# Performance work log

Hardware: AMD Instinct MI355X
Metric: run time of the kernel (lower is better)

The kernel has to match this reference:

```python
import jax, jax.numpy as jnp
import numpy as np

B, S, H, L = 8, 4096, 768, 256   # batch, seq_len, hidden_size, num_lines (= line_ids.max()+1)
ATT_HID = 1024                    # attention MLP hidden dim from nn.Linear(hidden,1024)


def setup_inputs() -> dict:
    key = jax.random.key(0)
    k0, k1, k2, k3 = jax.random.split(key, 4)
    token_hidden = jax.random.normal(k0, (B, S, H), dtype=jnp.float32)
    line_ids = jax.random.randint(k1, (B, S), 0, L)  # all valid; -1 would mark invalid
    W1 = jax.random.normal(k2, (H, ATT_HID), dtype=jnp.float32) * 0.02
    b1 = jnp.zeros((ATT_HID,), jnp.float32)
    W2 = jax.random.normal(k3, (ATT_HID, 1), dtype=jnp.float32) * 0.02
    b2 = jnp.zeros((1,), jnp.float32)
    return {"token_hidden": token_hidden, "line_ids": line_ids,
            "W1": W1, "b1": b1, "W2": W2, "b2": b2}


def reference(token_hidden, line_ids, W1, b1, W2, b2):
    b, s, h = token_hidden.shape
    num_lines = L
    n_seg = b * num_lines + 1  # last segment is a dump slot for invalid (-1) tokens

    # attention scores: Linear -> tanh -> Linear, squeeze(-1)  [b, s]
    scores = (jnp.tanh(token_hidden @ W1 + b1) @ W2 + b2)[..., 0]

    valid = (line_ids >= 0).reshape(-1)                                   # [b*s]
    seg = jnp.where(line_ids >= 0,
                    jnp.arange(b)[:, None] * num_lines + line_ids,
                    b * num_lines).reshape(-1)                            # [b*s]
    s_flat = jnp.where(valid, scores.reshape(-1), -jnp.inf)

    # segment-wise stable softmax
    m = jax.ops.segment_max(s_flat, seg, num_segments=n_seg)
    m = jnp.where(jnp.isfinite(m), m, 0.0)  # empty segments -> safe 0
    e = jnp.where(valid, jnp.exp(scores.reshape(-1) - m[seg]), 0.0)
    denom = jax.ops.segment_sum(e, seg, num_segments=n_seg)
    w = e / jnp.maximum(denom[seg], 1e-20)                                # [b*s]

    # weighted sum of tokens per (batch, line) segment
    feats = jax.ops.segment_sum(token_hidden.reshape(-1, h) * w[:, None],
                                seg, num_segments=n_seg)
    line_features = feats[: b * num_lines].reshape(b, num_lines, h)

    counts = jax.ops.segment_sum(valid.astype(jnp.float32), seg, num_segments=n_seg)
    line_mask = counts[: b * num_lines].reshape(b, num_lines) > 0
    return line_features, line_mask
```

## Files before the change

kernel.cpp:

```cpp
#include <hip/hip_runtime.h>
#include <hip/hip_bf16.h>
#include <string.h>

#define M_TOK 32768
#define H_DIM 768
#define AH    1024
#define NSEG  2048
#define LCAP  192
#define CONV_BLOCKS 12288

typedef __attribute__((ext_vector_type(8))) __bf16 bf16x8;
typedef __attribute__((ext_vector_type(4))) float f32x4;

__device__ __forceinline__ float tanh_fast(float x) {
  float e = __expf(2.0f * x);
  return 1.0f - 2.0f * __builtin_amdgcn_rcpf(e + 1.0f);
}

__device__ __forceinline__ float bf2f(unsigned short u) {
  unsigned int v = (unsigned int)u << 16;
  float f;
  memcpy(&f, &v, 4);
  return f;
}

__global__ __launch_bounds__(256) void prep_kernel(
    const float* __restrict__ W1, __hip_bfloat16* __restrict__ W1t,
    const float4* __restrict__ X4, uint4* __restrict__ Xb4) {
  __shared__ float tile[32][33];
  if (blockIdx.x < 768) {
    int nt = blockIdx.x & 31, ktile = blockIdx.x >> 5;
    int n0 = nt * 32, k0 = ktile * 32;
    int tx = threadIdx.x & 31, ty = threadIdx.x >> 5;
    for (int r = ty; r < 32; r += 8)
      tile[r][tx] = W1[(size_t)(k0 + r) * AH + n0 + tx];
    __syncthreads();
    for (int r = ty; r < 32; r += 8)
      W1t[(size_t)(n0 + r) * H_DIM + k0 + tx] = __float2bfloat16(tile[tx][r]);
  } else {
    int i = (blockIdx.x - 768) * 256 + threadIdx.x;
    float4 v0 = X4[i * 2];
    float4 v1 = X4[i * 2 + 1];
    __hip_bfloat16 h[8] = {
        __float2bfloat16(v0.x), __float2bfloat16(v0.y),
        __float2bfloat16(v0.z), __float2bfloat16(v0.w),
        __float2bfloat16(v1.x), __float2bfloat16(v1.y),
        __float2bfloat16(v1.z), __float2bfloat16(v1.w)};
    uint4 p;
    memcpy(&p, h, 16);
    Xb4[i] = p;
  }
}

__global__ __launch_bounds__(256) void attn_score_kernel(
    const __hip_bfloat16* __restrict__ Xbg,
    const __hip_bfloat16* __restrict__ W1tg, const float* __restrict__ b1g,
    const float* __restrict__ W2g, float* __restrict__ scores2) {
  __shared__ __align__(16) __bf16 As[128 * 64];
  __shared__ __align__(16) __bf16 Bs[128 * 64];

  const int tid = threadIdx.x;
  const int bid = blockIdx.x;
  const int xcd = bid & 7;
  const int s   = bid >> 3;
  const int m0  = (xcd * 32 + (s >> 3)) * 128;
  const int nt  = s & 7;
  const int n0  = nt * 128;
  const int lane = tid & 63;
  const int wave = tid >> 6;
  const int wm   = (wave >> 1) * 64;
  const int wn   = (wave & 1) * 64;
  const int ml   = lane & 15;
  const int gsw  = lane & 7;

  const __bf16* Xb = (const __bf16*)Xbg;
  const __bf16* W  = (const __bf16*)W1tg;

  const int srow = tid >> 3;
  const int scol = ((tid & 7) ^ (srow & 7)) * 8;

  f32x4 acc[4][4];
#pragma unroll
  for (int i = 0; i < 4; i++)
#pragma unroll
    for (int j = 0; j < 4; j++) acc[i][j] = (f32x4)0.f;

  for (int kt = 0; kt < H_DIM; kt += 64) {
#pragma unroll
    for (int p = 0; p < 4; ++p) {
      const __bf16* ga = Xb + (size_t)(m0 + p * 32 + srow) * H_DIM + kt + scol;
      __builtin_amdgcn_global_load_lds(
          (const __attribute__((address_space(1))) void*)ga,
          (__attribute__((address_space(3))) void*)&As[p * 2048 + tid * 8],
          16, 0, 0);
      const __bf16* gb = W + (size_t)(n0 + p * 32 + srow) * H_DIM + kt + scol;
      __builtin_amdgcn_global_load_lds(
          (const __attribute__((address_space(1))) void*)gb,
          (__attribute__((address_space(3))) void*)&Bs[p * 2048 + tid * 8],
          16, 0, 0);
    }
    __syncthreads();

#pragma unroll
    for (int c = 0; c < 2; ++c) {
      const int gq = c * 4 + (lane >> 4);
      const int gp = (gq ^ gsw) * 8;
      bf16x8 af[4], bf[4];
#pragma unroll
      for (int i = 0; i < 4; i++)
        af[i] = *(const bf16x8*)&As[(wm + i * 16 + ml) * 64 + gp];
#pragma unroll
      for (int j = 0; j < 4; j++)
        bf[j] = *(const bf16x8*)&Bs[(wn + j * 16 + ml) * 64 + gp];

#pragma unroll
      for (int i = 0; i < 4; i++)
#pragma unroll
        for (int j = 0; j < 4; j++)
          acc[i][j] = __builtin_amdgcn_mfma_f32_16x16x32_bf16(af[i], bf[j],
                                                              acc[i][j], 0, 0, 0);
    }
    __syncthreads();
  }

  float b1v[4], w2v[4];
#pragma unroll
  for (int j = 0; j < 4; j++) {
    int n = n0 + wn + j * 16 + ml;
    b1v[j] = b1g[n];
    w2v[j] = W2g[n];
  }
  const int q4 = (lane >> 4) * 4;
  float tval[4][4];
#pragma unroll
  for (int i = 0; i < 4; i++) {
#pragma unroll
    for (int p = 0; p < 4; p++) {
      float t = 0.f;
#pragma unroll
      for (int j = 0; j < 4; j++)
        t += tanh_fast(acc[i][j][p] + b1v[j]) * w2v[j];
      t += __shfl_xor(t, 1);
      t += __shfl_xor(t, 2);
      t += __shfl_xor(t, 4);
      t += __shfl_xor(t, 8);
      tval[i][p] = t;
    }
  }
  float* redbuf = (float*)As;
  if ((wave & 1) && ml == 0) {
#pragma unroll
    for (int i = 0; i < 4; i++)
#pragma unroll
      for (int p = 0; p < 4; p++)
        redbuf[wm + i * 16 + q4 + p] = tval[i][p];
  }
  __syncthreads();
  if (!(wave & 1) && ml == 0) {
#pragma unroll
    for (int i = 0; i < 4; i++)
#pragma unroll
      for (int p = 0; p < 4; p++) {
        int row = wm + i * 16 + q4 + p;
        scores2[(size_t)(m0 + row) * 8 + nt] = tval[i][p] + redbuf[row];
      }
  }
}

__global__ __launch_bounds__(256) void aggregate_kernel(
    const ushort* __restrict__ Xb, const float* __restrict__ scores2,
    const int* __restrict__ line_ids, float4* __restrict__ out4,
    float* __restrict__ out_mask) {
  __shared__ int   slist[LCAP];
  __shared__ float sw[LCAP];
  __shared__ int   wvc[4];
  __shared__ float wred[4];
  const int seg = blockIdx.x;
  const int b = seg >> 8, lid = seg & 255;
  const int tid = threadIdx.x, lane = tid & 63, wave = tid >> 6;
  const int base = b * 4096;

  int ids[16];
#pragma unroll
  for (int c = 0; c < 16; ++c) ids[c] = line_ids[base + c * 256 + tid];

  int total = 0;
#pragma unroll
  for (int c = 0; c < 16; ++c) {
    bool match = (ids[c] == lid);
    unsigned long long mask = __ballot(match);
    if (lane == 0) wvc[wave] = __popcll(mask);
    __syncthreads();
    int off = total;
    for (int w = 0; w < wave; ++w) off += wvc[w];
    if (match) {
      int pos = off + __popcll(mask & ((1ull << lane) - 1ull));
      if (pos < LCAP) slist[pos] = base + c * 256 + tid;
    }
    total += wvc[0] + wvc[1] + wvc[2] + wvc[3];
    __syncthreads();
  }
  int cnt = total > LCAP ? LCAP : total;
  if (tid == 0) out_mask[seg] = cnt > 0 ? 1.f : 0.f;
  if (cnt == 0) {
    if (tid < H_DIM / 4)
      out4[(size_t)seg * (H_DIM / 4) + tid] = make_float4(0.f, 0.f, 0.f, 0.f);
    return;
  }
  float lmax = -3.4e38f;
  if (tid < cnt) {
    const float4* sp = (const float4*)(scores2 + (size_t)slist[tid] * 8);
    float4 a = sp[0], c4 = sp[1];
    float sc = ((a.x + a.y) + (a.z + a.w)) + ((c4.x + c4.y) + (c4.z + c4.w));
    sw[tid] = sc;
    lmax = sc;
  }
#pragma unroll
  for (int d = 1; d < 64; d <<= 1) lmax = fmaxf(lmax, __shfl_xor(lmax, d));
  if (lane == 0) wred[wave] = lmax;
  __syncthreads();
  float m = fmaxf(fmaxf(wred[0], wred[1]), fmaxf(wred[2], wred[3]));
  float lsum = 0.f;
  if (tid < cnt) {
    float e = __expf(sw[tid] - m);
    sw[tid] = e;
    lsum = e;
  }
#pragma unroll
  for (int d = 1; d < 64; d <<= 1) lsum += __shfl_xor(lsum, d);
  __syncthreads();
  if (lane == 0) wred[wave] = lsum;
  __syncthreads();
  float denom = wred[0] + wred[1] + wred[2] + wred[3];
  float inv = __builtin_amdgcn_rcpf(fmaxf(denom, 1e-20f));
  if (tid < cnt) sw[tid] *= inv;
  __syncthreads();
  if (tid < H_DIM / 4) {
    const ushort4* xb = (const ushort4*)Xb + tid;
    float4 acc = make_float4(0.f, 0.f, 0.f, 0.f);
    int t = 0;
    for (; t + 4 <= cnt; t += 4) {
      ushort4 u0 = xb[(size_t)slist[t]     * (H_DIM / 4)];
      ushort4 u1 = xb[(size_t)slist[t + 1] * (H_DIM / 4)];
      ushort4 u2 = xb[(size_t)slist[t + 2] * (H_DIM / 4)];
      ushort4 u3 = xb[(size_t)slist[t + 3] * (H_DIM / 4)];
      float w0 = sw[t], w1 = sw[t + 1], w2 = sw[t + 2], w3 = sw[t + 3];
      acc.x += w0 * bf2f(u0.x) + w1 * bf2f(u1.x) + w2 * bf2f(u2.x) + w3 * bf2f(u3.x);
      acc.y += w0 * bf2f(u0.y) + w1 * bf2f(u1.y) + w2 * bf2f(u2.y) + w3 * bf2f(u3.y);
      acc.z += w0 * bf2f(u0.z) + w1 * bf2f(u1.z) + w2 * bf2f(u2.z) + w3 * bf2f(u3.z);
      acc.w += w0 * bf2f(u0.w) + w1 * bf2f(u1.w) + w2 * bf2f(u2.w) + w3 * bf2f(u3.w);
    }
    for (; t < cnt; ++t) {
      ushort4 u = xb[(size_t)slist[t] * (H_DIM / 4)];
      float w = sw[t];
      acc.x += w * bf2f(u.x); acc.y += w * bf2f(u.y);
      acc.z += w * bf2f(u.z); acc.w += w * bf2f(u.w);
    }
    out4[(size_t)seg * (H_DIM / 4) + tid] = acc;
  }
}

extern "C" void kernel_launch(void* const* d_in, const int* in_sizes, int n_in,
                              void* d_out, int out_size, void* d_ws, size_t ws_size,
                              hipStream_t stream) {
  const float* X        = (const float*)d_in[0];
  const int*   line_ids = (const int*)d_in[1];
  const float* W1       = (const float*)d_in[2];
  const float* b1       = (const float*)d_in[3];
  const float* W2       = (const float*)d_in[4];

  char* p = (char*)d_ws;
  __hip_bfloat16* Xb      = (__hip_bfloat16*)p;  p += (size_t)M_TOK * H_DIM * 2;
  __hip_bfloat16* W1t     = (__hip_bfloat16*)p;  p += 1572864;
  float*          scores2 = (float*)p;           p += (size_t)M_TOK * 8 * 4;

  float* out_feats = (float*)d_out;
  float* out_mask  = out_feats + (size_t)NSEG * H_DIM;

  prep_kernel<<<768 + CONV_BLOCKS, 256, 0, stream>>>(
      W1, W1t, (const float4*)X, (uint4*)Xb);
  attn_score_kernel<<<2048, 256, 0, stream>>>(Xb, W1t, b1, W2, scores2);
  aggregate_kernel<<<NSEG, 256, 0, stream>>>((const ushort*)Xb, scores2,
                                             line_ids, (float4*)out_feats,
                                             out_mask);
}
```

Measured before the change: 249.2 us.

## Rewrite score GEMM as 256x256 tile with double-buffered LDS pipeline

The attention-score GEMM moves from 128x128 tiles with 256 threads to 256x256 tiles with 512 threads and 8 waves. LDS is double-buffered so next-k global-to-LDS loads are issued in four phases interleaved with MFMA work, using explicit vmcnt waits, sched barriers and setprio. The larger N tile halves the partial score columns from 8 to 4, and the aggregate kernel reads correspondingly less. The cost is higher register and LDS pressure (128KB LDS per block, occupancy 2 requested) and fewer blocks, 512, to spread across the CUs.

```diff
diff --git a/kernel.cpp b/kernel.cpp
--- a/kernel.cpp
+++ b/kernel.cpp
@@ -8,6 +8,7 @@
 #define NSEG  2048
 #define LCAP  192
 #define CONV_BLOCKS 12288
+#define NKT   12
 
 typedef __attribute__((ext_vector_type(8))) __bf16 bf16x8;
 typedef __attribute__((ext_vector_type(4))) float f32x4;
@@ -52,118 +53,150 @@
   }
 }
 
-__global__ __launch_bounds__(256) void attn_score_kernel(
+#define WAITV(N) asm volatile("s_waitcnt vmcnt(" #N ")" ::: "memory")
+#define WAITL0   asm volatile("s_waitcnt lgkmcnt(0)" ::: "memory")
+
+__global__ __launch_bounds__(512, 2) void attn_score_kernel(
     const __hip_bfloat16* __restrict__ Xbg,
     const __hip_bfloat16* __restrict__ W1tg, const float* __restrict__ b1g,
     const float* __restrict__ W2g, float* __restrict__ scores2) {
-  __shared__ __align__(16) __bf16 As[128 * 64];
-  __shared__ __align__(16) __bf16 Bs[128 * 64];
+  __shared__ __align__(16) __bf16 As[2][256 * 64];
+  __shared__ __align__(16) __bf16 Bs[2][256 * 64];
 
   const int tid = threadIdx.x;
   const int bid = blockIdx.x;
   const int xcd = bid & 7;
-  const int s   = bid >> 3;
-  const int m0  = (xcd * 32 + (s >> 3)) * 128;
-  const int nt  = s & 7;
-  const int n0  = nt * 128;
+  const int sq  = bid >> 3;
+  const int m0  = (xcd * 16 + (sq >> 2)) * 256;
+  const int ntl = sq & 3;
+  const int n0  = ntl * 256;
   const int lane = tid & 63;
   const int wave = tid >> 6;
-  const int wm   = (wave >> 1) * 64;
-  const int wn   = (wave & 1) * 64;
+  const int wm   = wave >> 2;
+  const int wx   = wave & 3;
   const int ml   = lane & 15;
-  const int gsw  = lane & 7;
+  const int lh   = lane >> 4;
 
   const __bf16* Xb = (const __bf16*)Xbg;
   const __bf16* W  = (const __bf16*)W1tg;
 
-  const int srow = tid >> 3;
-  const int scol = ((tid & 7) ^ (srow & 7)) * 8;
-
-  f32x4 acc[4][4];
-#pragma unroll
-  for (int i = 0; i < 4; i++)
-#pragma unroll
-    for (int j = 0; j < 4; j++) acc[i][j] = (f32x4)0.f;
-
-  for (int kt = 0; kt < H_DIM; kt += 64) {
-#pragma unroll
-    for (int p = 0; p < 4; ++p) {
-      const __bf16* ga = Xb + (size_t)(m0 + p * 32 + srow) * H_DIM + kt + scol;
-      __builtin_amdgcn_global_load_lds(
-          (const __attribute__((address_space(1))) void*)ga,
-          (__attribute__((address_space(3))) void*)&As[p * 2048 + tid * 8],
-          16, 0, 0);
-      const __bf16* gb = W + (size_t)(n0 + p * 32 + srow) * H_DIM + kt + scol;
-      __builtin_amdgcn_global_load_lds(
-          (const __attribute__((address_space(1))) void*)gb,
-          (__attribute__((address_space(3))) void*)&Bs[p * 2048 + tid * 8],
-          16, 0, 0);
+  const int lr   = tid >> 3;
+  const int scol = ((tid & 7) ^ (lr & 7)) << 3;
+
+  int aRow[4], bRow[4];
+#pragma unroll
+  for (int q = 0; q < 4; ++q) {
+    aRow[q] = m0 + ((q & 1) << 7) + ((q >> 1) << 6) + lr;
+    int lrow = (q << 6) + lr;
+    bRow[q] = n0 + (((lrow >> 5) & 3) << 6) + ((lrow >> 7) << 5) + (lrow & 31);
+  }
+
+  f32x4 acc[8][4];
+#pragma unroll
+  for (int i = 0; i < 8; ++i)
+#pragma unroll
+    for (int j = 0; j < 4; ++j) acc[i][j] = (f32x4)0.f;
+
+#define STAGE_A(q, buf, kt)                                                    \
+  __builtin_amdgcn_global_load_lds(                                            \
+      (const __attribute__((address_space(1))) void*)(Xb +                     \
+          (size_t)aRow[q] * H_DIM + (kt) + scol),                              \
+      (__attribute__((address_space(3))) void*)&As[buf][(q) * 4096 + tid * 8], \
+      16, 0, 0)
+#define STAGE_B(q, buf, kt)                                                    \
+  __builtin_amdgcn_global_load_lds(                                            \
+      (const __attribute__((address_space(1))) void*)(W +                      \
+          (size_t)bRow[q] * H_DIM + (kt) + scol),                              \
+      (__attribute__((address_space(3))) void*)&Bs[buf][(q) * 4096 + tid * 8], \
+      16, 0, 0)
+
+  STAGE_A(0, 0, 0); STAGE_A(1, 0, 0);
+  STAGE_B(0, 0, 0); STAGE_B(1, 0, 0);
+  STAGE_A(2, 0, 0); STAGE_A(3, 0, 0);
+  STAGE_B(2, 0, 0); STAGE_B(3, 0, 0);
+
+#define PHASE_BODY(Q, P, SS)                                                   \
+  {                                                                            \
+    __builtin_amdgcn_s_barrier();                                              \
+    __builtin_amdgcn_sched_barrier(0);                                         \
+    const int mh = (Q) & 1, nh = (Q) >> 1;                                     \
+    bf16x8 af[4][2], bfr[2][2];                                                \
+    _Pragma("unroll") for (int lf = 0; lf < 4; ++lf) {                         \
+      int ra = (mh << 7) + (wm << 6) + (lf << 4) + ml;                         \
+      _Pragma("unroll") for (int kk = 0; kk < 2; ++kk) {                       \
+        int ph = ((kk << 2) + lh) ^ (ml & 7);                                  \
+        af[lf][kk] = *(const bf16x8*)&As[P][(ra << 6) + (ph << 3)];            \
+      }                                                                        \
+    }                                                                          \
+    _Pragma("unroll") for (int jj = 0; jj < 2; ++jj) {                         \
+      int rb = (nh << 7) + (wx << 5) + (jj << 4) + ml;                         \
+      _Pragma("unroll") for (int kk = 0; kk < 2; ++kk) {                       \
+        int ph = ((kk << 2) + lh) ^ (ml & 7);                                  \
+        bfr[jj][kk] = *(const bf16x8*)&Bs[P][(rb << 6) + (ph << 3)];           \
+      }                                                                        \
+    }                                                                          \
+    SS;                                                                        \
+    WAITL0;                                                                    \
+    __builtin_amdgcn_sched_barrier(0);                                         \
+    __builtin_amdgcn_s_setprio(1);                                             \
+    _Pragma("unroll") for (int lf = 0; lf < 4; ++lf)                           \
+      _Pragma("unroll") for (int jj = 0; jj < 2; ++jj)                         \
+        _Pragma("unroll") for (int kk = 0; kk < 2; ++kk)                       \
+          acc[mh * 4 + lf][nh * 2 + jj] =                                      \
+              __builtin_amdgcn_mfma_f32_16x16x32_bf16(                         \
+                  af[lf][kk], bfr[jj][kk], acc[mh * 4 + lf][nh * 2 + jj],      \
+                  0, 0, 0);                                                    \
+    __builtin_amdgcn_s_setprio(0);                                             \
+  }
+
+  int p = 0;
+  for (int t = 0; t < NKT - 1; ++t) {
+    const int ktn = (t + 1) << 6;
+    WAITV(4);
+    PHASE_BODY(0, p, { STAGE_A(0, p ^ 1, ktn); STAGE_A(1, p ^ 1, ktn); });
+    WAITV(4);
+    PHASE_BODY(1, p, { STAGE_B(0, p ^ 1, ktn); STAGE_B(1, p ^ 1, ktn); });
+    WAITV(4);
+    PHASE_BODY(2, p, { STAGE_A(2, p ^ 1, ktn); STAGE_A(3, p ^ 1, ktn); });
+    PHASE_BODY(3, p, { STAGE_B(2, p ^ 1, ktn); STAGE_B(3, p ^ 1, ktn); });
+    p ^= 1;
+  }
+  WAITV(4);
+  PHASE_BODY(0, p, ((void)0));
+  WAITV(2);
+  PHASE_BODY(1, p, ((void)0));
+  WAITV(0);
+  PHASE_BODY(2, p, ((void)0));
+  PHASE_BODY(3, p, ((void)0));
+
+  float b1v[4], w2v[4];
+#pragma unroll
+  for (int nf = 0; nf < 4; ++nf) {
+    int n = n0 + wx * 64 + nf * 16 + ml;
+    b1v[nf] = b1g[n];
+    w2v[nf] = W2g[n];
+  }
+  float* red = (float*)&As[0][0];
+#pragma unroll
+  for (int mf = 0; mf < 8; ++mf) {
+#pragma unroll
+    for (int pp = 0; pp < 4; ++pp) {
+      float tsum = 0.f;
+#pragma unroll
+      for (int nf = 0; nf < 4; ++nf)
+        tsum += tanh_fast(acc[mf][nf][pp] + b1v[nf]) * w2v[nf];
+      tsum += __shfl_xor(tsum, 1);
+      tsum += __shfl_xor(tsum, 2);
+      tsum += __shfl_xor(tsum, 4);
+      tsum += __shfl_xor(tsum, 8);
+      if (ml == 0)
+        red[wx * 256 + wm * 128 + mf * 16 + lh * 4 + pp] = tsum;
     }
-    __syncthreads();
-
-#pragma unroll
-    for (int c = 0; c < 2; ++c) {
-      const int gq = c * 4 + (lane >> 4);
-      const int gp = (gq ^ gsw) * 8;
-      bf16x8 af[4], bf[4];
-#pragma unroll
-      for (int i = 0; i < 4; i++)
-        af[i] = *(const bf16x8*)&As[(wm + i * 16 + ml) * 64 + gp];
-#pragma unroll
-      for (int j = 0; j < 4; j++)
-        bf[j] = *(const bf16x8*)&Bs[(wn + j * 16 + ml) * 64 + gp];
-
-#pragma unroll
-      for (int i = 0; i < 4; i++)
-#pragma unroll
-        for (int j = 0; j < 4; j++)
-          acc[i][j] = __builtin_amdgcn_mfma_f32_16x16x32_bf16(af[i], bf[j],
-                                                              acc[i][j], 0, 0, 0);
-    }
-    __syncthreads();
-  }
-
-  float b1v[4], w2v[4];
-#pragma unroll
-  for (int j = 0; j < 4; j++) {
-    int n = n0 + wn + j * 16 + ml;
-    b1v[j] = b1g[n];
-    w2v[j] = W2g[n];
-  }
-  const int q4 = (lane >> 4) * 4;
-  float tval[4][4];
-#pragma unroll
-  for (int i = 0; i < 4; i++) {
-#pragma unroll
-    for (int p = 0; p < 4; p++) {
-      float t = 0.f;
-#pragma unroll
-      for (int j = 0; j < 4; j++)
-        t += tanh_fast(acc[i][j][p] + b1v[j]) * w2v[j];
-      t += __shfl_xor(t, 1);
-      t += __shfl_xor(t, 2);
-      t += __shfl_xor(t, 4);
-      t += __shfl_xor(t, 8);
-      tval[i][p] = t;
-    }
-  }
-  float* redbuf = (float*)As;
-  if ((wave & 1) && ml == 0) {
-#pragma unroll
-    for (int i = 0; i < 4; i++)
-#pragma unroll
-      for (int p = 0; p < 4; p++)
-        redbuf[wm + i * 16 + q4 + p] = tval[i][p];
-  }
-  __syncthreads();
-  if (!(wave & 1) && ml == 0) {
-#pragma unroll
-    for (int i = 0; i < 4; i++)
-#pragma unroll
-      for (int p = 0; p < 4; p++) {
-        int row = wm + i * 16 + q4 + p;
-        scores2[(size_t)(m0 + row) * 8 + nt] = tval[i][p] + redbuf[row];
-      }
+  }
+  __syncthreads();
+  if (tid < 256) {
+    float v = (red[tid] + red[256 + tid]) + (red[512 + tid] + red[768 + tid]);
+    scores2[(size_t)(m0 + tid) * 4 + ntl] = v;
   }
 }
 
@@ -209,9 +242,8 @@
   }
   float lmax = -3.4e38f;
   if (tid < cnt) {
-    const float4* sp = (const float4*)(scores2 + (size_t)slist[tid] * 8);
-    float4 a = sp[0], c4 = sp[1];
-    float sc = ((a.x + a.y) + (a.z + a.w)) + ((c4.x + c4.y) + (c4.z + c4.w));
+    const float4 a = *(const float4*)(scores2 + (size_t)slist[tid] * 4);
+    float sc = (a.x + a.y) + (a.z + a.w);
     sw[tid] = sc;
     lmax = sc;
   }
@@ -272,14 +304,14 @@
   char* p = (char*)d_ws;
   __hip_bfloat16* Xb      = (__hip_bfloat16*)p;  p += (size_t)M_TOK * H_DIM * 2;
   __hip_bfloat16* W1t     = (__hip_bfloat16*)p;  p += 1572864;
-  float*          scores2 = (float*)p;           p += (size_t)M_TOK * 8 * 4;
+  float*          scores2 = (float*)p;           p += (size_t)M_TOK * 4 * 4;
 
   float* out_feats = (float*)d_out;
   float* out_mask  = out_feats + (size_t)NSEG * H_DIM;
 
   prep_kernel<<<768 + CONV_BLOCKS, 256, 0, stream>>>(
       W1, W1t, (const float4*)X, (uint4*)Xb);
-  attn_score_kernel<<<2048, 256, 0, stream>>>(Xb, W1t, b1, W2, scores2);
+  attn_score_kernel<<<512, 512, 0, stream>>>(Xb, W1t, b1, W2, scores2);
   aggregate_kernel<<<NSEG, 256, 0, stream>>>((const ushort*)Xb, scores2,
                                              line_ids, (float4*)out_feats,
                                              out_mask);
```

Result: faster. 233.0 us (-6.5%).
